# Performance work log

Measured on AMD Instinct MI355X. Metric: run time of the kernel, lower is better.

Reference implementation:

```python
import jax, jax.numpy as jnp
import numpy as np

FX, FY, CX, CY = 320.0, 320.0, 320.0, 240.0
N_MP, N_KF, M = 200000, 2000, 4000000


def setup_inputs() -> dict:
    key = jax.random.key(0)
    k1, k2, k3, k4 = jax.random.split(key, 4)
    # Map-point positions; shift to [1,2) so the homogeneous z after the (near-identity)
    # pose transform stays well away from zero for a stable perspective divide.
    tMP = jax.random.uniform(k1, (N_MP, 3), dtype=jnp.float32) + 1.0
    # Keyframe poses: identity + small perturbation (realistic SE3-like 4x4 matrices).
    tKF = jnp.eye(4, dtype=jnp.float32)[None] + 0.05 * jax.random.normal(k2, (N_KF, 4, 4), dtype=jnp.float32)
    # Measurement edges: (kf_id, mp_id) pairs.
    kf_ids = jax.random.randint(k3, (M,), 0, N_KF, dtype=jnp.int32)
    mp_ids = jax.random.randint(k4, (M,), 0, N_MP, dtype=jnp.int32)
    # Unique, sorted id columns (MPs[:,0] / KFs[:,0] in the original module).
    idxKF = jnp.arange(N_KF, dtype=jnp.int32)
    idxMP = jnp.arange(N_MP, dtype=jnp.int32)
    return {"tMP": tMP, "tKF": tKF, "kf_ids": kf_ids, "mp_ids": mp_ids,
            "idxKF": idxKF, "idxMP": idxMP}


def reference(tMP, tKF, kf_ids, mp_ids, idxKF, idxMP):
    # ID match. Original builds an O(M*N) boolean equality tensor and takes
    # torch.where(...)[1]; for unique sorted id arrays this is exactly a
    # sorted-index lookup, so we use searchsorted (same result, no huge temp).
    indexKF = jnp.searchsorted(idxKF, kf_ids)   # [M]
    indexMP = jnp.searchsorted(idxMP, mp_ids)   # [M]
    # Homogeneous map points: pad with 1 (F.pad(..., value=1) in original).
    tMPhomo = jnp.concatenate([tMP, jnp.ones((tMP.shape[0], 1), tMP.dtype)], axis=1)  # [N_MP,4]
    # Gather per-edge pose / point and do batched 4x4 @ 4 matvec.
    P = jnp.einsum('mij,mj->mi', tKF[indexKF], tMPhomo[indexMP])  # [M,4]
    # Perspective divide + intrinsics.
    ptx = P[:, 0] / P[:, 2] * FX + CX
    pty = P[:, 1] / P[:, 2] * FY + CY
    return jnp.stack([ptx, pty], axis=1)  # [M,2]
```

## Files before the change

### kernel.cpp

```cpp
#include <hip/hip_runtime.h>


#define FX_ 320.0f
#define FY_ 320.0f
#define CX_ 320.0f
#define CY_ 240.0f

__global__ __launch_bounds__(256) void ba_project_kernel(
    const float* __restrict__ tMP,
    const float* __restrict__ tKF,
    const int*   __restrict__ kf_ids,
    const int*   __restrict__ mp_ids,
    float* __restrict__ out,
    int M)
{
    int t = blockIdx.x * blockDim.x + threadIdx.x;
    int m0 = t * 4;
    if (m0 + 3 < M) {
        int4 kf4 = *reinterpret_cast<const int4*>(kf_ids + m0);
        int4 mp4 = *reinterpret_cast<const int4*>(mp_ids + m0);
        int kf[4] = {kf4.x, kf4.y, kf4.z, kf4.w};
        int mp[4] = {mp4.x, mp4.y, mp4.z, mp4.w};
        float res[8];
        #pragma unroll
        for (int i = 0; i < 4; ++i) {
            const float* K = tKF + (size_t)kf[i] * 16;
            float4 r0 = *reinterpret_cast<const float4*>(K + 0);
            float4 r1 = *reinterpret_cast<const float4*>(K + 4);
            float4 r2 = *reinterpret_cast<const float4*>(K + 8);
            const float* p = tMP + (size_t)mp[i] * 3;
            float x = p[0], y = p[1], z = p[2];
            float P0 = fmaf(r0.x, x, fmaf(r0.y, y, fmaf(r0.z, z, r0.w)));
            float P1 = fmaf(r1.x, x, fmaf(r1.y, y, fmaf(r1.z, z, r1.w)));
            float P2 = fmaf(r2.x, x, fmaf(r2.y, y, fmaf(r2.z, z, r2.w)));
            float inv = 1.0f / P2;
            res[2 * i + 0] = fmaf(P0 * inv, FX_, CX_);
            res[2 * i + 1] = fmaf(P1 * inv, FY_, CY_);
        }
        float4* o = reinterpret_cast<float4*>(out + (size_t)m0 * 2);
        o[0] = make_float4(res[0], res[1], res[2], res[3]);
        o[1] = make_float4(res[4], res[5], res[6], res[7]);
    } else {
        for (int m = m0; m < M; ++m) {
            int kf = kf_ids[m];
            int mp = mp_ids[m];
            const float* K = tKF + (size_t)kf * 16;
            float4 r0 = *reinterpret_cast<const float4*>(K + 0);
            float4 r1 = *reinterpret_cast<const float4*>(K + 4);
            float4 r2 = *reinterpret_cast<const float4*>(K + 8);
            const float* p = tMP + (size_t)mp * 3;
            float x = p[0], y = p[1], z = p[2];
            float P0 = fmaf(r0.x, x, fmaf(r0.y, y, fmaf(r0.z, z, r0.w)));
            float P1 = fmaf(r1.x, x, fmaf(r1.y, y, fmaf(r1.z, z, r1.w)));
            float P2 = fmaf(r2.x, x, fmaf(r2.y, y, fmaf(r2.z, z, r2.w)));
            float inv = 1.0f / P2;
            out[2 * (size_t)m + 0] = fmaf(P0 * inv, FX_, CX_);
            out[2 * (size_t)m + 1] = fmaf(P1 * inv, FY_, CY_);
        }
    }
}

extern "C" void kernel_launch(void* const* d_in, const int* in_sizes, int n_in,
                              void* d_out, int out_size, void* d_ws, size_t ws_size,
                              hipStream_t stream) {
    const float* tMP    = (const float*)d_in[0];
    const float* tKF    = (const float*)d_in[1];
    const int*   kf_ids = (const int*)d_in[2];
    const int*   mp_ids = (const int*)d_in[3];
    float* out = (float*)d_out;
    int M = in_sizes[2];

    int threads = (M + 3) / 4;
    int block = 256;
    int grid = (threads + block - 1) / block;
    ba_project_kernel<<<grid, block, 0, stream>>>(tMP, tKF, kf_ids, mp_ids, out, M);
}
```

Before: 136.2 us.

## Stage keyframe poses in LDS and pad map points to float4

Adds a pre-pass that repacks map points into an aligned float4 workspace so each gather becomes a single 16-byte load. Each 1024-thread block copies the first three rows of all keyframe poses (96 KB) into shared memory, so per-edge pose reads hit LDS instead of scattered global loads. The per-block LDS fill costs time, occupancy drops to one block per CU, and an extra kernel launch plus a workspace write are added. A direct fallback kernel runs when the workspace is too small or there are too many keyframes.

Measured after the change: 123.9 us. 9.0% less time.

```diff
diff --git a/kernel.cpp b/kernel.cpp
--- a/kernel.cpp
+++ b/kernel.cpp
@@ -6,33 +6,56 @@
 #define CX_ 320.0f
 #define CY_ 240.0f
 
-__global__ __launch_bounds__(256) void ba_project_kernel(
-    const float* __restrict__ tMP,
-    const float* __restrict__ tKF,
-    const int*   __restrict__ kf_ids,
-    const int*   __restrict__ mp_ids,
+#define MAX_KF 2000
+#define MAIN_BLOCK 1024
+
+__global__ __launch_bounds__(256) void mp_pack_kernel(
+    const float* __restrict__ tMP, float4* __restrict__ tMPh, int N)
+{
+    int i = blockIdx.x * blockDim.x + threadIdx.x;
+    if (i < N) {
+        const float* p = tMP + (size_t)i * 3;
+        tMPh[i] = make_float4(p[0], p[1], p[2], 1.0f);
+    }
+}
+
+__global__ __launch_bounds__(MAIN_BLOCK) void ba_project_lds_kernel(
+    const float4* __restrict__ tMPh,
+    const float*  __restrict__ tKF,
+    const int*    __restrict__ kf_ids,
+    const int*    __restrict__ mp_ids,
     float* __restrict__ out,
-    int M)
+    int M, int N_KF)
 {
-    int t = blockIdx.x * blockDim.x + threadIdx.x;
+    __shared__ float4 sKF[MAX_KF * 3];
+
+    int nChunks = N_KF * 3;
+    for (int i = threadIdx.x; i < nChunks; i += MAIN_BLOCK) {
+        int k = i / 3;
+        int r = i - k * 3;
+        sKF[i] = *reinterpret_cast<const float4*>(tKF + (size_t)k * 16 + r * 4);
+    }
+    __syncthreads();
+
+    int t = blockIdx.x * MAIN_BLOCK + threadIdx.x;
     int m0 = t * 4;
     if (m0 + 3 < M) {
         int4 kf4 = *reinterpret_cast<const int4*>(kf_ids + m0);
         int4 mp4 = *reinterpret_cast<const int4*>(mp_ids + m0);
         int kf[4] = {kf4.x, kf4.y, kf4.z, kf4.w};
         int mp[4] = {mp4.x, mp4.y, mp4.z, mp4.w};
+        float4 p[4];
+        #pragma unroll
+        for (int i = 0; i < 4; ++i) p[i] = tMPh[mp[i]];
         float res[8];
         #pragma unroll
         for (int i = 0; i < 4; ++i) {
-            const float* K = tKF + (size_t)kf[i] * 16;
-            float4 r0 = *reinterpret_cast<const float4*>(K + 0);
-            float4 r1 = *reinterpret_cast<const float4*>(K + 4);
-            float4 r2 = *reinterpret_cast<const float4*>(K + 8);
-            const float* p = tMP + (size_t)mp[i] * 3;
-            float x = p[0], y = p[1], z = p[2];
-            float P0 = fmaf(r0.x, x, fmaf(r0.y, y, fmaf(r0.z, z, r0.w)));
-            float P1 = fmaf(r1.x, x, fmaf(r1.y, y, fmaf(r1.z, z, r1.w)));
-            float P2 = fmaf(r2.x, x, fmaf(r2.y, y, fmaf(r2.z, z, r2.w)));
+            float4 r0 = sKF[kf[i] * 3 + 0];
+            float4 r1 = sKF[kf[i] * 3 + 1];
+            float4 r2 = sKF[kf[i] * 3 + 2];
+            float P0 = fmaf(r0.x, p[i].x, fmaf(r0.y, p[i].y, fmaf(r0.z, p[i].z, r0.w)));
+            float P1 = fmaf(r1.x, p[i].x, fmaf(r1.y, p[i].y, fmaf(r1.z, p[i].z, r1.w)));
+            float P2 = fmaf(r2.x, p[i].x, fmaf(r2.y, p[i].y, fmaf(r2.z, p[i].z, r2.w)));
             float inv = 1.0f / P2;
             res[2 * i + 0] = fmaf(P0 * inv, FX_, CX_);
             res[2 * i + 1] = fmaf(P1 * inv, FY_, CY_);
@@ -43,20 +66,43 @@
     } else {
         for (int m = m0; m < M; ++m) {
             int kf = kf_ids[m];
-            int mp = mp_ids[m];
-            const float* K = tKF + (size_t)kf * 16;
-            float4 r0 = *reinterpret_cast<const float4*>(K + 0);
-            float4 r1 = *reinterpret_cast<const float4*>(K + 4);
-            float4 r2 = *reinterpret_cast<const float4*>(K + 8);
-            const float* p = tMP + (size_t)mp * 3;
-            float x = p[0], y = p[1], z = p[2];
-            float P0 = fmaf(r0.x, x, fmaf(r0.y, y, fmaf(r0.z, z, r0.w)));
-            float P1 = fmaf(r1.x, x, fmaf(r1.y, y, fmaf(r1.z, z, r1.w)));
-            float P2 = fmaf(r2.x, x, fmaf(r2.y, y, fmaf(r2.z, z, r2.w)));
+            float4 p = tMPh[mp_ids[m]];
+            float4 r0 = sKF[kf * 3 + 0];
+            float4 r1 = sKF[kf * 3 + 1];
+            float4 r2 = sKF[kf * 3 + 2];
+            float P0 = fmaf(r0.x, p.x, fmaf(r0.y, p.y, fmaf(r0.z, p.z, r0.w)));
+            float P1 = fmaf(r1.x, p.x, fmaf(r1.y, p.y, fmaf(r1.z, p.z, r1.w)));
+            float P2 = fmaf(r2.x, p.x, fmaf(r2.y, p.y, fmaf(r2.z, p.z, r2.w)));
             float inv = 1.0f / P2;
             out[2 * (size_t)m + 0] = fmaf(P0 * inv, FX_, CX_);
             out[2 * (size_t)m + 1] = fmaf(P1 * inv, FY_, CY_);
         }
+    }
+}
+
+__global__ __launch_bounds__(256) void ba_project_direct_kernel(
+    const float* __restrict__ tMP, const float* __restrict__ tKF,
+    const int* __restrict__ kf_ids, const int* __restrict__ mp_ids,
+    float* __restrict__ out, int M)
+{
+    int t = blockIdx.x * blockDim.x + threadIdx.x;
+    int m0 = t * 4;
+    int mEnd = (m0 + 4 < M) ? (m0 + 4) : M;
+    for (int m = m0; m < mEnd; ++m) {
+        int kf = kf_ids[m];
+        int mp = mp_ids[m];
+        const float* K = tKF + (size_t)kf * 16;
+        float4 r0 = *reinterpret_cast<const float4*>(K + 0);
+        float4 r1 = *reinterpret_cast<const float4*>(K + 4);
+        float4 r2 = *reinterpret_cast<const float4*>(K + 8);
+        const float* p = tMP + (size_t)mp * 3;
+        float x = p[0], y = p[1], z = p[2];
+        float P0 = fmaf(r0.x, x, fmaf(r0.y, y, fmaf(r0.z, z, r0.w)));
+        float P1 = fmaf(r1.x, x, fmaf(r1.y, y, fmaf(r1.z, z, r1.w)));
+        float P2 = fmaf(r2.x, x, fmaf(r2.y, y, fmaf(r2.z, z, r2.w)));
+        float inv = 1.0f / P2;
+        out[2 * (size_t)m + 0] = fmaf(P0 * inv, FX_, CX_);
+        out[2 * (size_t)m + 1] = fmaf(P1 * inv, FY_, CY_);
     }
 }
 
@@ -68,10 +114,22 @@
     const int*   kf_ids = (const int*)d_in[2];
     const int*   mp_ids = (const int*)d_in[3];
     float* out = (float*)d_out;
-    int M = in_sizes[2];
+    int M    = in_sizes[2];
+    int N_MP = in_sizes[0] / 3;
+    int N_KF = in_sizes[1] / 16;
 
-    int threads = (M + 3) / 4;
-    int block = 256;
-    int grid = (threads + block - 1) / block;
-    ba_project_kernel<<<grid, block, 0, stream>>>(tMP, tKF, kf_ids, mp_ids, out, M);
+    size_t need_ws = (size_t)N_MP * sizeof(float4);
+    if (N_KF <= MAX_KF && ws_size >= need_ws) {
+        float4* tMPh = (float4*)d_ws;
+        mp_pack_kernel<<<(N_MP + 255) / 256, 256, 0, stream>>>(tMP, tMPh, N_MP);
+        int threads = (M + 3) / 4;
+        int grid = (threads + MAIN_BLOCK - 1) / MAIN_BLOCK;
+        ba_project_lds_kernel<<<grid, MAIN_BLOCK, 0, stream>>>(
+            tMPh, tKF, kf_ids, mp_ids, out, M, N_KF);
+    } else {
+        int threads = (M + 3) / 4;
+        int grid = (threads + 255) / 256;
+        ba_project_direct_kernel<<<grid, 256, 0, stream>>>(
+            tMP, tKF, kf_ids, mp_ids, out, M);
+    }
 }
```
